# Optimization experiments

Hardware: AMD Instinct MI355X
Metric: run time of the kernel (lower is better)

Reference implementation:

```python
import jax, jax.numpy as jnp
import numpy as np

B, V, T, CIN, WEMB, H, NW = 32, 500, 24, 2, 4, 64, 8
C0 = CIN + WEMB  # 6 channels entering first layer


def _stglstm(x, supports, Wg, bg, Wo, bo, out_len=None, final_layer=False):
    # x: (B, C, V, T); supports: (S, V, V)
    Bb, C, Vv, Tt = x.shape
    T_steps = out_len if out_len is not None else Tt
    if final_layer:
        xs = jnp.broadcast_to(x[:, :, :, -1][None], (T_steps, Bb, C, Vv))
    else:
        xs = jnp.moveaxis(x, 3, 0)  # (T, B, C, V)

    def step(carry, xt):
        hx, cx = carry
        comb = xt + hx  # (B, C, V)
        feats = [comb]
        for s in range(supports.shape[0]):  # fixed small support_len loop
            x1 = jnp.einsum('bcv,vw->bcw', comb, supports[s])
            x2 = jnp.einsum('bcv,vw->bcw', x1, supports[s])
            feats += [x1, x2]  # order-2 diffusion
        g = jnp.concatenate(feats, axis=1)  # (B, 7C, V)
        gates = jnp.einsum('bgv,og->bov', g, Wg) + bg[None, :, None]  # (B, 4C, V)
        i, f, cg, o = jnp.split(gates, 4, axis=1)
        cy = jax.nn.sigmoid(f) * cx + jax.nn.sigmoid(i) * cg  # cellgate is linear (no tanh), as in source
        hy = jax.nn.sigmoid(o) * jnp.tanh(cy)
        return (hy, cy), hy

    h0 = jnp.zeros((Bb, C, Vv), x.dtype)
    _, hs = jax.lax.scan(step, (h0, h0), xs)  # hs: (T, B, C, V)
    hs = jnp.moveaxis(hs, 0, 3)  # (B, C, V, T)
    return jnp.einsum('bcvt,oc->bovt', hs, Wo) + bo[None, :, None, None]


def _se(x, Wa, Wb):
    y = x.mean(axis=(2, 3))  # (B, C) global avg pool
    y = jax.nn.sigmoid(jax.nn.relu(y @ Wa.T) @ Wb.T)
    return x * y[:, :, None, None]


def setup_inputs():
    key = jax.random.key(0)
    ks = jax.random.split(key, 24)

    def n(k, shape, s=0.05):
        return jax.random.normal(k, shape, jnp.float32) * s

    A = jax.random.uniform(ks[0], (3, V, V), jnp.float32)
    A = A / A.sum(-1, keepdims=True)  # row-stochastic random-walk matrices
    return {
        'x': n(ks[1], (B, CIN, V, T), 1.0),
        'supports': A,
        'w_type': jax.random.randint(ks[2], (B, V, T), 0, NW, dtype=jnp.int32),
        'Wemb': n(ks[3], (NW, WEMB)),
        'Wg0': n(ks[4], (4 * C0, 7 * C0)), 'bg0': jnp.zeros((4 * C0,), jnp.float32),
        'Wo0': n(ks[5], (H, C0)), 'bo0': jnp.zeros((H,), jnp.float32),
        'Ws0a': n(ks[6], (H // 16, H)), 'Ws0b': n(ks[7], (H, H // 16)),
        'Wg1': n(ks[8], (4 * H, 7 * H)), 'bg1': jnp.zeros((4 * H,), jnp.float32),
        'Wo1': n(ks[9], (H, H)), 'bo1': jnp.zeros((H,), jnp.float32),
        'Ws1a': n(ks[10], (H // 16, H)), 'Ws1b': n(ks[11], (H, H // 16)),
        'Wg2': n(ks[12], (4 * H, 7 * H)), 'bg2': jnp.zeros((4 * H,), jnp.float32),
        'Wo2': n(ks[13], (H, H)), 'bo2': jnp.zeros((H,), jnp.float32),
        'Wg3': n(ks[14], (4 * H, 7 * H)), 'bg3': jnp.zeros((4 * H,), jnp.float32),
        'Wo3': n(ks[15], (2, H)), 'bo3': jnp.zeros((2,), jnp.float32),
    }


def reference(x, supports, w_type, Wemb, Wg0, bg0, Wo0, bo0, Ws0a, Ws0b,
              Wg1, bg1, Wo1, bo1, Ws1a, Ws1b, Wg2, bg2, Wo2, bo2,
              Wg3, bg3, Wo3, bo3):
    w_vec = Wemb[w_type]  # (B, V, T, wemb)
    w_vec = jnp.transpose(w_vec, (0, 3, 1, 2))  # (B, wemb, V, T)
    h = jnp.concatenate([x, w_vec], axis=1)  # (B, CIN+wemb, V, T)
    h = _stglstm(h, supports, Wg0, bg0, Wo0, bo0)
    h = _se(h, Ws0a, Ws0b)
    h = _stglstm(h, supports, Wg1, bg1, Wo1, bo1)
    h = _se(h, Ws1a, Ws1b)
    h = _stglstm(h, supports, Wg2, bg2, Wo2, bo2)
    out = _stglstm(h, supports, Wg3, bg3, Wo3, bo3, out_len=T, final_layer=True)
    return out  # (B, 2, V, out_len)
```

## Files before the change

### kernel.cpp

```cpp
#include <hip/hip_runtime.h>
#include <math.h>

#define NV 500
#define NB 32
#define NT 24
#define NH 64

typedef _Float16 f16;
typedef _Float16 f16x8 __attribute__((ext_vector_type(8)));
typedef _Float16 f16x4 __attribute__((ext_vector_type(4)));
typedef float    f32x4 __attribute__((ext_vector_type(4)));

__device__ __forceinline__ float sigm(float x){ return 1.f/(1.f+expf(-x)); }

__global__ void k_a2(const float* __restrict__ A, float* __restrict__ A2)
{
    int idx = blockIdx.x*256 + threadIdx.x;
    if (idx >= 3*500*500) return;
    int wv = idx % 500; int rest = idx/500; int r = rest % 500; int s = rest/500;
    const float* Ar = A + ((size_t)s*500 + r)*500;
    const float* Ac = A + (size_t)s*500*500 + wv;
    float a = 0.f;
    for (int u = 0; u < 500; u++) a += Ar[u]*Ac[(size_t)u*500];
    A2[idx] = a;
}

__global__ void k_acat(const float* __restrict__ A, const float* __restrict__ A2,
                       f16* __restrict__ AcatT)
{
    int idx = blockIdx.x*256 + threadIdx.x;
    if (idx >= 3072*512) return;
    int k = idx & 511;
    int n = idx >> 9;
    int j = n >> 9, wv = n & 511;
    float val = 0.f;
    if (k < 500 && wv < 500) {
        int s = j >> 1;
        const float* M = (j & 1) ? A2 : A;
        val = M[((size_t)s*500 + k)*500 + wv];
    }
    AcatT[idx] = (f16)val;
}

__global__ void k_f2h(const float* __restrict__ src, f16* __restrict__ dst, int n)
{
    int idx = blockIdx.x*256 + threadIdx.x;
    if (idx < n) dst[idx] = (f16)src[idx];
}

__global__ __launch_bounds__(256)
void k_diff(const f16* __restrict__ Acv, const f16* __restrict__ Bt,
            f16* __restrict__ fout, int Mtot, int C, int G)
{
    __shared__ f16 lA[128*32];
    __shared__ f16 lB[128*32];
    const int tid = threadIdx.x;
    const int n0 = blockIdx.x*128, m0 = blockIdx.y*128;
    const int r0 = tid>>2, c0 = tid&3;
    const int swz0 = r0*32 + ((c0 ^ ((r0>>1)&3))<<3);
    const int swz1 = swz0 + 64*32;
    int mA0 = m0 + r0;      if (mA0 > Mtot-1) mA0 = Mtot-1;
    int mA1 = m0 + r0 + 64; if (mA1 > Mtot-1) mA1 = Mtot-1;
    const f16* gA0 = Acv + (size_t)mA0*512 + c0*8;
    const f16* gA1 = Acv + (size_t)mA1*512 + c0*8;
    const f16* gB0 = Bt + (size_t)(n0+r0)*512 + c0*8;
    const f16* gB1 = Bt + (size_t)(n0+r0+64)*512 + c0*8;

    const int w = tid>>6, lane = tid&63;
    const int wr = (w>>1)<<6, wc = (w&1)<<6;
    const int fm = lane&15, fk = lane>>4;
    const int fch = (fk ^ ((fm>>1)&3))<<3;

    f32x4 acc[4][4];
    #pragma unroll
    for (int i=0;i<4;i++)
        #pragma unroll
        for (int j=0;j<4;j++) acc[i][j] = (f32x4){0.f,0.f,0.f,0.f};

    f32x4 ra0 = *(const f32x4*)gA0, ra1 = *(const f32x4*)gA1;
    f32x4 rb0 = *(const f32x4*)gB0, rb1 = *(const f32x4*)gB1;

    for (int ks = 0; ks < 16; ks++) {
        __syncthreads();
        *(f32x4*)(lA + swz0) = ra0;  *(f32x4*)(lA + swz1) = ra1;
        *(f32x4*)(lB + swz0) = rb0;  *(f32x4*)(lB + swz1) = rb1;
        if (ks < 15) {
            int o = (ks+1)*32;
            ra0 = *(const f32x4*)(gA0 + o); ra1 = *(const f32x4*)(gA1 + o);
            rb0 = *(const f32x4*)(gB0 + o); rb1 = *(const f32x4*)(gB1 + o);
        }
        __syncthreads();
        f16x8 af[4], bf[4];
        #pragma unroll
        for (int i=0;i<4;i++) af[i] = *(const f16x8*)(lA + (wr + i*16 + fm)*32 + fch);
        #pragma unroll
        for (int j=0;j<4;j++) bf[j] = *(const f16x8*)(lB + (wc + j*16 + fm)*32 + fch);
        #pragma unroll
        for (int i=0;i<4;i++)
            #pragma unroll
            for (int j=0;j<4;j++)
                acc[i][j] = __builtin_amdgcn_mfma_f32_16x16x32_f16(af[i], bf[j], acc[i][j], 0, 0, 0);
    }

    #pragma unroll
    for (int j=0;j<4;j++) {
        int col = n0 + wc + j*16 + fm;
        int jb = col >> 9, wv = col & 511;
        if (wv >= 500) continue;
        #pragma unroll
        for (int i=0;i<4;i++) {
            int mb = m0 + wr + i*16 + fk*4;
            if (C == 64) {
                if (mb >= Mtot) continue;
                int b = mb >> 6, c = mb & 63;
                f16x4 h4;
                h4[0]=(f16)acc[i][j][0]; h4[1]=(f16)acc[i][j][1];
                h4[2]=(f16)acc[i][j][2]; h4[3]=(f16)acc[i][j][3];
                *(f16x4*)(fout + ((size_t)b*512 + wv)*G + C + jb*C + c) = h4;
            } else {
                #pragma unroll
                for (int r=0;r<4;r++) {
                    int m = mb + r;
                    if (m < Mtot) {
                        int b = m / C, c = m - b*C;
                        fout[((size_t)b*512 + wv)*G + C + jb*C + c] = (f16)acc[i][j][r];
                    }
                }
            }
        }
    }
}

__global__ __launch_bounds__(256)
void k_gateslstm(const f16* __restrict__ fT, const f16* __restrict__ Wg,
                 const float* __restrict__ bg, float* __restrict__ cst,
                 const f16* __restrict__ Xn, f16* __restrict__ hsave,
                 const float* __restrict__ Wo3, const float* __restrict__ bo3,
                 float* __restrict__ out, int t,
                 f16* __restrict__ fTout, f16* __restrict__ ccv,
                 int first, int writecomb)
{
    __shared__ f16 lA[64*32];
    __shared__ f16 lB[256*32];
    __shared__ float ExF[4*64*65];
    __shared__ float bgS[256];
    __shared__ f16 combS[64*68];
    const int tid = threadIdx.x;
    const int m0 = blockIdx.x*64, b = blockIdx.y;
    const f16* Ab = fT + (size_t)b*512*448;
    bgS[tid] = bg[tid];

    const int r0 = tid>>2, c0 = tid&3;
    const int swz = r0*32 + ((c0 ^ ((r0>>1)&3))<<3);
    const f16* gA = Ab + (size_t)(m0+r0)*448 + c0*8;
    const f16* gB = Wg + (size_t)r0*448 + c0*8;

    const int w = tid>>6, lane = tid&63;
    const int wc = w<<6;
    const int fm = lane&15, fk = lane>>4;
    const int fch = (fk ^ ((fm>>1)&3))<<3;

    f32x4 acc[4][4];
    #pragma unroll
    for (int i=0;i<4;i++)
        #pragma unroll
        for (int j=0;j<4;j++) acc[i][j] = (f32x4){0.f,0.f,0.f,0.f};

    f32x4 ra  = *(const f32x4*)gA;
    f32x4 rb0 = *(const f32x4*)gB;
    f32x4 rb1 = *(const f32x4*)(gB + (size_t)64*448);
    f32x4 rb2 = *(const f32x4*)(gB + (size_t)128*448);
    f32x4 rb3 = *(const f32x4*)(gB + (size_t)192*448);

    for (int ks = 0; ks < 14; ks++) {
        __syncthreads();
        *(f32x4*)(lA + swz) = ra;
        *(f32x4*)(lB + swz)          = rb0;
        *(f32x4*)(lB + 64*32 + swz)  = rb1;
        *(f32x4*)(lB + 128*32 + swz) = rb2;
        *(f32x4*)(lB + 192*32 + swz) = rb3;
        if (ks < 13) {
            int o = (ks+1)*32;
            ra  = *(const f32x4*)(gA + o);
            rb0 = *(const f32x4*)(gB + o);
            rb1 = *(const f32x4*)(gB + (size_t)64*448 + o);
            rb2 = *(const f32x4*)(gB + (size_t)128*448 + o);
            rb3 = *(const f32x4*)(gB + (size_t)192*448 + o);
        }
        __syncthreads();
        f16x8 af[4], bf[4];
        #pragma unroll
        for (int i=0;i<4;i++) af[i] = *(const f16x8*)(lA + (i*16 + fm)*32 + fch);
        #pragma unroll
        for (int j=0;j<4;j++) bf[j] = *(const f16x8*)(lB + (wc + j*16 + fm)*32 + fch);
        #pragma unroll
        for (int i=0;i<4;i++)
            #pragma unroll
            for (int j=0;j<4;j++)
                acc[i][j] = __builtin_amdgcn_mfma_f32_16x16x32_f16(af[i], bf[j], acc[i][j], 0, 0, 0);
    }

    __syncthreads();
    #pragma unroll
    for (int i=0;i<4;i++)
        #pragma unroll
        for (int j=0;j<4;j++)
            #pragma unroll
            for (int r=0;r<4;r++)
                ExF[((w<<6) + i*16 + (fk<<2) + r)*65 + (j<<4) + fm] = acc[i][j][r];
    __syncthreads();

    const int vl = tid>>2, p = tid&3;
    const int v = m0 + vl;
    const size_t row = (size_t)b*512 + v;
    float hy[16];
    float* cp = cst + row*64 + (p<<4);
    #pragma unroll
    for (int k4=0;k4<4;k4++) {
        f32x4 cx4 = first ? (f32x4){0.f,0.f,0.f,0.f} : *(const f32x4*)(cp + k4*4);
        f32x4 cy4;
        #pragma unroll
        for (int e=0;e<4;e++) {
            int c = (p<<4) + k4*4 + e;
            float gi = ExF[(         vl)*65 + c] + bgS[c];
            float gf = ExF[( 64 +    vl)*65 + c] + bgS[64+c];
            float gc = ExF[(128 +    vl)*65 + c] + bgS[128+c];
            float go = ExF[(192 +    vl)*65 + c] + bgS[192+c];
            float cy = sigm(gf)*cx4[e] + sigm(gi)*gc;
            cy4[e] = cy;
            hy[k4*4+e] = sigm(go)*tanhf(cy);
        }
        *(f32x4*)(cp + k4*4) = cy4;
    }

    if (hsave) {
        alignas(16) f16 tmp[16];
        #pragma unroll
        for (int k=0;k<16;k++) tmp[k] = (f16)hy[k];
        f16* hp = hsave + row*64 + (p<<4);
        *(f32x4*)hp = *(f32x4*)tmp;
        *(f32x4*)(hp+8) = *(f32x4*)(tmp+8);
    }

    if (out) {
        float r0s = 0.f, r1s = 0.f;
        #pragma unroll
        for (int k=0;k<16;k++){ r0s += Wo3[(p<<4)+k]*hy[k]; r1s += Wo3[64+(p<<4)+k]*hy[k]; }
        r0s += __shfl_xor(r0s, 1, 64); r0s += __shfl_xor(r0s, 2, 64);
        r1s += __shfl_xor(r1s, 1, 64); r1s += __shfl_xor(r1s, 2, 64);
        if (p == 0 && v < 500) {
            out[((size_t)(b*2+0)*500 + v)*24 + t] = r0s + bo3[0];
            out[((size_t)(b*2+1)*500 + v)*24 + t] = r1s + bo3[1];
        }
    }

    if (writecomb) {
        alignas(16) f16 c16[16];
        if (v < 500) {
            const f16* xp = Xn + row*64 + (p<<4);
            alignas(16) f16 xv[16];
            *(f32x4*)xv = *(const f32x4*)xp;
            *(f32x4*)(xv+8) = *(const f32x4*)(xp+8);
            #pragma unroll
            for (int k=0;k<16;k++) c16[k] = (f16)((float)xv[k] + hy[k]);
        } else {
            #pragma unroll
            for (int k=0;k<16;k++) c16[k] = (f16)0.f;
        }
        f16* fp = fTout + row*448 + (p<<4);
        *(f32x4*)fp = *(f32x4*)c16;
        *(f32x4*)(fp+8) = *(f32x4*)(c16+8);
        #pragma unroll
        for (int k=0;k<16;k++) combS[vl*68 + (p<<4) + k] = c16[k];
        __syncthreads();
        const int c = tid>>2, jj = tid&3;
        alignas(16) f16 tmp[16];
        #pragma unroll
        for (int k=0;k<16;k++) tmp[k] = combS[(jj*16+k)*68 + c];
        f16* dst = ccv + ((size_t)b*64 + c)*512 + m0 + jj*16;
        *(f32x4*)dst = *(f32x4*)tmp;
        *(f32x4*)(dst+8) = *(f32x4*)(tmp+8);
    }
}

__global__ __launch_bounds__(256)
void k_seed(const f16* __restrict__ X0, f16* __restrict__ fT, f16* __restrict__ ccv)
{
    __shared__ f16 combS[64*68];
    const int b = blockIdx.y, v0 = blockIdx.x*64;
    const int tid = threadIdx.x, vl = tid>>2, p = tid&3;
    const int v = v0 + vl;
    const size_t row = (size_t)b*512 + v;
    alignas(16) f16 c16[16];
    if (v < 500) {
        const f16* xp = X0 + row*64 + p*16;
        *(f32x4*)c16 = *(const f32x4*)xp;
        *(f32x4*)(c16+8) = *(const f32x4*)(xp+8);
    } else {
        #pragma unroll
        for (int k=0;k<16;k++) c16[k] = (f16)0.f;
    }
    f16* fp = fT + row*448 + p*16;
    *(f32x4*)fp = *(f32x4*)c16;
    *(f32x4*)(fp+8) = *(f32x4*)(c16+8);
    #pragma unroll
    for (int k=0;k<16;k++) combS[vl*68 + p*16 + k] = c16[k];
    __syncthreads();
    const int c = tid>>2, j = tid&3;
    alignas(16) f16 tmp[16];
    #pragma unroll
    for (int k=0;k<16;k++) tmp[k] = combS[(j*16+k)*68 + c];
    f16* dst = ccv + ((size_t)b*64 + c)*512 + v0 + j*16;
    *(f32x4*)dst = *(f32x4*)tmp;
    *(f32x4*)(dst+8) = *(f32x4*)(tmp+8);
}

__global__ __launch_bounds__(256)
void k_xprojm(const f16* __restrict__ src, const f16* __restrict__ WoF,
              const float* __restrict__ bo, const float* __restrict__ se,
              f16* __restrict__ X)
{
    __shared__ f16 lA[128*64];
    __shared__ f16 lB[64*64];
    const int tid = threadIdx.x;
    const size_t m0 = (size_t)blockIdx.x*128;
    const int r0 = tid>>2, c0 = tid&3;
    const int swz = r0*32 + ((c0 ^ ((r0>>1)&3))<<3);
    const f16* gA0 = src + (m0 + r0)*64 + c0*8;
    const f16* gA1 = gA0 + 64*64;
    const f16* gB  = WoF + r0*64 + c0*8;

    *(f32x4*)(lA + swz)               = *(const f32x4*)gA0;
    *(f32x4*)(lA + 2048 + swz)        = *(const f32x4*)gA1;
    *(f32x4*)(lA + 4096 + swz)        = *(const f32x4*)(gA0 + 32);
    *(f32x4*)(lA + 6144 + swz)        = *(const f32x4*)(gA1 + 32);
    *(f32x4*)(lB + swz)               = *(const f32x4*)gB;
    *(f32x4*)(lB + 2048 + swz)        = *(const f32x4*)(gB + 32);
    __syncthreads();

    const int w = tid>>6, lane = tid&63;
    const int wr = w<<5;
    const int fm = lane&15, fk = lane>>4;
    const int fch = (fk ^ ((fm>>1)&3))<<3;

    f32x4 acc[2][4];
    #pragma unroll
    for (int i=0;i<2;i++)
        #pragma unroll
        for (int j=0;j<4;j++) acc[i][j] = (f32x4){0.f,0.f,0.f,0.f};

    #pragma unroll
    for (int ks=0; ks<2; ks++) {
        f16x8 af[2], bf[4];
        #pragma unroll
        for (int i=0;i<2;i++) af[i] = *(const f16x8*)(lA + ks*4096 + (wr + i*16 + fm)*32 + fch);
        #pragma unroll
        for (int j=0;j<4;j++) bf[j] = *(const f16x8*)(lB + ks*2048 + (j*16 + fm)*32 + fch);
        #pragma unroll
        for (int i=0;i<2;i++)
            #pragma unroll
            for (int j=0;j<4;j++)
                acc[i][j] = __builtin_amdgcn_mfma_f32_16x16x32_f16(af[i], bf[j], acc[i][j], 0, 0, 0);
    }
    __syncthreads();

    const int bb = (int)((m0 >> 9) & 31);
    #pragma unroll
    for (int j=0;j<4;j++) {
        const int c = (j<<4) + fm;
        const float bias = bo[c];
        const float sf = se ? se[bb*64 + c] : 1.f;
        #pragma unroll
        for (int i=0;i<2;i++) {
            const int rbase = wr + i*16 + (fk<<2);
            #pragma unroll
            for (int r=0;r<4;r++)
                lA[(rbase + r)*64 + c] = (f16)(sf*(acc[i][j][r] + bias));
        }
    }
    __syncthreads();
    #pragma unroll
    for (int pass=0; pass<4; pass++) {
        int chunk = pass*256 + tid;
        int row = chunk>>3, off = (chunk&7)<<3;
        *(f32x4*)(X + (m0 + row)*64 + off) = *(const f32x4*)(lA + row*64 + off);
    }
}

__global__ void k_xproj1(const float* __restrict__ src, const float* __restrict__ Wo,
                         const float* __restrict__ bo, const float* __restrict__ se,
                         f16* __restrict__ X, int total)
{
    int id = blockIdx.x*256 + threadIdx.x;
    if (id >= total) return;
    int c = id & 63;
    size_t row = (size_t)(id >> 6);
    int b = (int)((row >> 9) & 31);
    const float* sp = src + row*6;
    float a = bo[c];
    #pragma unroll
    for (int j=0;j<6;j++) a += Wo[c*6+j]*sp[j];
    X[id] = (f16)(se[b*64+c]*a);
}

__global__ void k_xe(const float* __restrict__ x, const int* __restrict__ wt,
                     const float* __restrict__ Wemb, float* __restrict__ XE)
{
    int id = blockIdx.x*256 + threadIdx.x;
    if (id >= NT*NB*512) return;
    int v = id & 511; int r = id >> 9; int b = r & 31; int t = r >> 5;
    float vals[6] = {0.f,0.f,0.f,0.f,0.f,0.f};
    if (v < 500) {
        vals[0] = x[((size_t)(b*2+0)*500 + v)*24 + t];
        vals[1] = x[((size_t)(b*2+1)*500 + v)*24 + t];
        int wty = wt[((size_t)b*500 + v)*24 + t];
        vals[2] = Wemb[wty*4+0]; vals[3] = Wemb[wty*4+1];
        vals[4] = Wemb[wty*4+2]; vals[5] = Wemb[wty*4+3];
    }
    float* xe = XE + (size_t)id*6;
    #pragma unroll
    for (int c = 0; c < 6; c++) xe[c] = vals[c];
}

__global__ void k_seed0(const float* __restrict__ XE, f16* __restrict__ f0T,
                        f16* __restrict__ ccv0)
{
    int id = blockIdx.x*256 + threadIdx.x;
    if (id >= NB*512) return;
    int v = id & 511, b = id >> 9;
    const float* xe = XE + (size_t)id*6;
    #pragma unroll
    for (int c = 0; c < 6; c++) {
        f16 h = (v < 500) ? (f16)xe[c] : (f16)0.f;
        f0T[(size_t)id*42 + c] = h;
        ccv0[((size_t)b*6 + c)*512 + v] = h;
    }
}

__global__ __launch_bounds__(256)
void k_glstm0(f16* f0T, const float* __restrict__ Wg0,
              const float* __restrict__ bg0, float* __restrict__ cst0,
              float* __restrict__ hs0T, const float* __restrict__ XE,
              f16* __restrict__ ccv0, int t)
{
    __shared__ float WgS[24*42];
    __shared__ float bgS[24];
    int tid = threadIdx.x;
    for (int i = tid; i < 24*42; i += 256) WgS[i] = Wg0[i];
    if (tid < 24) bgS[tid] = bg0[tid];
    __syncthreads();
    int id = blockIdx.x*256 + tid;
    if (id >= NB*500) return;
    int b = id / 500, v = id - b*500;
    const f16* fp = f0T + ((size_t)b*512 + v)*42;
    float fv[42];
    #pragma unroll
    for (int g = 0; g < 42; g++) fv[g] = (float)fp[g];
    float gates[24];
    #pragma unroll
    for (int o = 0; o < 24; o++) {
        float a = bgS[o];
        #pragma unroll
        for (int g = 0; g < 42; g++) a += WgS[o*42+g]*fv[g];
        gates[o] = a;
    }
    size_t hrow = (((size_t)t*NB + b)*512 + v)*6;
    const float* xe = XE + (((size_t)(t+1)*NB + b)*512 + v)*6;
    #pragma unroll
    for (int c = 0; c < 6; c++) {
        size_t ci = ((size_t)b*500 + v)*6 + c;
        float cx = t ? cst0[ci] : 0.f;
        float cy = sigm(gates[6+c])*cx + sigm(gates[c])*gates[12+c];
        cst0[ci] = cy;
        float h = sigm(gates[18+c])*tanhf(cy);
        hs0T[hrow + c] = h;
        if (t < 23) {
            float cmb = xe[c] + h;
            f0T[((size_t)b*512 + v)*42 + c] = (f16)cmb;
            ccv0[((size_t)b*6 + c)*512 + v] = (f16)cmb;
        }
    }
}

__global__ void k_mean0(const float* __restrict__ hs0T, float* __restrict__ mean0)
{
    int b = blockIdx.x;
    float acc[6] = {0,0,0,0,0,0};
    for (int i = threadIdx.x; i < 24*500; i += 256) {
        int tt = i/500, v = i - tt*500;
        const float* p = hs0T + (((size_t)tt*NB + b)*512 + v)*6;
        #pragma unroll
        for (int c=0;c<6;c++) acc[c] += p[c];
    }
    __shared__ float red[256];
    for (int c=0;c<6;c++) {
        red[threadIdx.x] = acc[c]; __syncthreads();
        for (int s=128;s>0;s>>=1) { if (threadIdx.x<s) red[threadIdx.x]+=red[threadIdx.x+s]; __syncthreads(); }
        if (threadIdx.x==0) mean0[b*6+c] = red[0]/12000.f;
        __syncthreads();
    }
}

__global__ void k_mean1(const f16* __restrict__ hs1T, float* __restrict__ mean1)
{
    int cg = blockIdx.x, b = blockIdx.y;
    float acc[8] = {0,0,0,0,0,0,0,0};
    for (int i = threadIdx.x; i < 24*500; i += 256) {
        int tt = i/500, v = i - tt*500;
        const f16* p = hs1T + (((size_t)tt*NB + b)*512 + v)*64 + cg*8;
        #pragma unroll
        for (int c=0;c<8;c++) acc[c] += (float)p[c];
    }
    __shared__ float red[256];
    for (int c=0;c<8;c++) {
        red[threadIdx.x] = acc[c]; __syncthreads();
        for (int s=128;s>0;s>>=1) { if (threadIdx.x<s) red[threadIdx.x]+=red[threadIdx.x+s]; __syncthreads(); }
        if (threadIdx.x==0) mean1[b*64 + cg*8 + c] = red[0]/12000.f;
        __syncthreads();
    }
}

__global__ void k_se(const float* __restrict__ meanhs, const float* __restrict__ Wo,
                     const float* __restrict__ bo, int Cin,
                     const float* __restrict__ Wa, const float* __restrict__ Wb,
                     float* __restrict__ se)
{
    int b = blockIdx.x; int c = threadIdx.x;
    __shared__ float y[64]; __shared__ float a[4];
    float acc = bo[c];
    for (int j = 0; j < Cin; j++) acc += Wo[(size_t)c*Cin + j] * meanhs[b*Cin + j];
    y[c] = acc;
    __syncthreads();
    if (c < 4) {
        float s = 0.f;
        for (int j = 0; j < 64; j++) s += Wa[c*64 + j] * y[j];
        a[c] = fmaxf(s, 0.f);
    }
    __syncthreads();
    float s = 0.f;
    #pragma unroll
    for (int j = 0; j < 4; j++) s += Wb[c*4 + j] * a[j];
    se[b*64 + c] = 1.f/(1.f + expf(-s));
}

extern "C" void kernel_launch(void* const* d_in, const int* in_sizes, int n_in,
                              void* d_out, int out_size, void* d_ws, size_t ws_size,
                              hipStream_t stream)
{
    const float* x    = (const float*)d_in[0];
    const float* sup  = (const float*)d_in[1];
    const int*   wt   = (const int*)  d_in[2];
    const float* Wemb = (const float*)d_in[3];
    const float* Wg0  = (const float*)d_in[4];
    const float* bg0  = (const float*)d_in[5];
    const float* Wo0  = (const float*)d_in[6];
    const float* bo0  = (const float*)d_in[7];
    const float* Wa0  = (const float*)d_in[8];
    const float* Wb0  = (const float*)d_in[9];
    const float* Wg1  = (const float*)d_in[10];
    const float* bg1  = (const float*)d_in[11];
    const float* Wo1  = (const float*)d_in[12];
    const float* bo1  = (const float*)d_in[13];
    const float* Wa1  = (const float*)d_in[14];
    const float* Wb1  = (const float*)d_in[15];
    const float* Wg2  = (const float*)d_in[16];
    const float* bg2  = (const float*)d_in[17];
    const float* Wo2  = (const float*)d_in[18];
    const float* bo2  = (const float*)d_in[19];
    const float* Wg3  = (const float*)d_in[20];
    const float* bg3  = (const float*)d_in[21];
    const float* Wo3  = (const float*)d_in[22];
    const float* bo3  = (const float*)d_in[23];
    float* out = (float*)d_out;
    (void)in_sizes; (void)n_in; (void)out_size; (void)ws_size;

    char* ws = (char*)d_ws;
    size_t off = 0;
    f16*   AcatT  = (f16*)(ws + off);   off += (size_t)3072*512*2;
    float* A2     = (float*)(ws + off); off += (size_t)3*500*500*4;
    f16*   WgF1   = (f16*)(ws + off);   off += (size_t)256*448*2;
    f16*   WgF2   = (f16*)(ws + off);   off += (size_t)256*448*2;
    f16*   WgF3   = (f16*)(ws + off);   off += (size_t)256*448*2;
    f16*   WoF1   = (f16*)(ws + off);   off += (size_t)64*64*2;
    f16*   WoF2   = (f16*)(ws + off);   off += (size_t)64*64*2;
    f16*   comb_cv= (f16*)(ws + off);   off += (size_t)2048*512*2;
    f16*   ccv0   = (f16*)(ws + off);   off += (size_t)192*512*2;
    f16*   featsT = (f16*)(ws + off);   off += (size_t)NB*512*448*2;
    f16*   f0T    = (f16*)(ws + off);   off += (size_t)NB*512*42*2;
    float* XE     = (float*)(ws + off); off += (size_t)NT*NB*512*6*4;
    float* hs0T   = (float*)(ws + off); off += (size_t)NT*NB*512*6*4;
    f16*   hs1T   = (f16*)(ws + off);   off += (size_t)NT*NB*512*64*2;
    f16*   hT     = (f16*)(ws + off);   off += (size_t)NB*512*64*2;
    float* cstT   = (float*)(ws + off); off += (size_t)NB*512*64*4;
    float* cst0   = (float*)(ws + off); off += (size_t)NB*500*6*4;
    f16*   Xbuf   = (f16*)(ws + off);   off += (size_t)NT*NB*512*64*2;
    f16*   X3     = (f16*)(ws + off);   off += (size_t)NB*512*64*2;
    float* mean0  = (float*)(ws + off); off += 8192;
    float* se0    = (float*)(ws + off); off += 8192;
    float* mean1  = (float*)(ws + off); off += 8192;
    float* se1    = (float*)(ws + off); off += 8192;

    const size_t sliceH = (size_t)NB*512*64;

    k_a2  <<<(3*500*500 + 255)/256, 256, 0, stream>>>(sup, A2);
    k_acat<<<(3072*512 + 255)/256, 256, 0, stream>>>(sup, A2, AcatT);
    k_f2h <<<(256*448 + 255)/256, 256, 0, stream>>>(Wg1, WgF1, 256*448);
    k_f2h <<<(256*448 + 255)/256, 256, 0, stream>>>(Wg2, WgF2, 256*448);
    k_f2h <<<(256*448 + 255)/256, 256, 0, stream>>>(Wg3, WgF3, 256*448);
    k_f2h <<<16, 256, 0, stream>>>(Wo1, WoF1, 64*64);
    k_f2h <<<16, 256, 0, stream>>>(Wo2, WoF2, 64*64);
    k_xe  <<<(NT*NB*512)/256, 256, 0, stream>>>(x, wt, Wemb, XE);

    k_seed0<<<(NB*512)/256, 256, 0, stream>>>(XE, f0T, ccv0);
    for (int t = 0; t < NT; t++) {
        k_diff  <<<dim3(24, 2), 256, 0, stream>>>(ccv0, AcatT, f0T, 192, 6, 42);
        k_glstm0<<<(NB*500 + 255)/256, 256, 0, stream>>>(f0T, Wg0, bg0, cst0, hs0T, XE, ccv0, t);
    }
    k_mean0<<<NB, 256, 0, stream>>>(hs0T, mean0);
    k_se   <<<NB, 64, 0, stream>>>(mean0, Wo0, bo0, 6, Wa0, Wb0, se0);

    k_xproj1<<<(NT*NB*512*64)/256, 256, 0, stream>>>(hs0T, Wo0, bo0, se0, Xbuf, NT*NB*512*64);
    k_seed <<<dim3(8, NB), 256, 0, stream>>>(Xbuf, featsT, comb_cv);
    for (int t = 0; t < NT; t++) {
        k_diff <<<dim3(24, 16), 256, 0, stream>>>(comb_cv, AcatT, featsT, 2048, 64, 448);
        k_gateslstm<<<dim3(8, NB), 256, 0, stream>>>(featsT, WgF1, bg1, cstT,
                 (t < 23) ? Xbuf + (size_t)(t+1)*sliceH : (const f16*)nullptr,
                 hs1T + (size_t)t*sliceH, nullptr, nullptr, nullptr, t,
                 featsT, comb_cv, t == 0, t < 23);
    }
    k_mean1<<<dim3(8, NB), 256, 0, stream>>>(hs1T, mean1);
    k_se   <<<NB, 64, 0, stream>>>(mean1, Wo1, bo1, 64, Wa1, Wb1, se1);

    k_xprojm<<<(NT*NB*512)/128, 256, 0, stream>>>(hs1T, WoF1, bo1, se1, Xbuf);
    k_seed <<<dim3(8, NB), 256, 0, stream>>>(Xbuf, featsT, comb_cv);
    for (int t = 0; t < NT; t++) {
        k_diff <<<dim3(24, 16), 256, 0, stream>>>(comb_cv, AcatT, featsT, 2048, 64, 448);
        k_gateslstm<<<dim3(8, NB), 256, 0, stream>>>(featsT, WgF2, bg2, cstT,
                 (t < 23) ? Xbuf + (size_t)(t+1)*sliceH : (const f16*)nullptr,
                 (t == 23) ? hT : (f16*)nullptr, nullptr, nullptr, nullptr, t,
                 featsT, comb_cv, t == 0, t < 23);
    }

    k_xprojm<<<(NB*512)/128, 256, 0, stream>>>(hT, WoF2, bo2, nullptr, X3);
    k_seed <<<dim3(8, NB), 256, 0, stream>>>(X3, featsT, comb_cv);
    for (int t = 0; t < NT; t++) {
        k_diff <<<dim3(24, 16), 256, 0, stream>>>(comb_cv, AcatT, featsT, 2048, 64, 448);
        k_gateslstm<<<dim3(8, NB), 256, 0, stream>>>(featsT, WgF3, bg3, cstT,
                 X3, nullptr, Wo3, bo3, out, t,
                 featsT, comb_cv, t == 0, t < 23);
    }
}
```

Before: 4.593 ms.

## Fuse diffusion GEMM into gate LSTM kernel with ping-pong buffers, tile A2 precompute

Merges the per-step diffusion kernel and the gate/LSTM kernel into one k_step kernel. Each block computes its 64-node slice of the six diffused feature sets into shared memory, then runs the gate GEMM straight from LDS, so the 448-wide feature tensor no longer round-trips through global memory. This halves the launches per timestep, and ping-pong buffers for comb/ccv avoid read-write races across blocks. In exchange, each block recomputes diffusion over all 64 channels with only 256 blocks, which lowers parallelism compared with the separate 384-block diffusion kernel. Gate pre-activations are also staged in f16 rather than f32. The A^2 precompute is separately rewritten as a shared-memory tiled SGEMM.

```diff
diff --git a/kernel.cpp b/kernel.cpp
--- a/kernel.cpp
+++ b/kernel.cpp
@@ -13,16 +13,54 @@
 
 __device__ __forceinline__ float sigm(float x){ return 1.f/(1.f+expf(-x)); }
 
-__global__ void k_a2(const float* __restrict__ A, float* __restrict__ A2)
-{
-    int idx = blockIdx.x*256 + threadIdx.x;
-    if (idx >= 3*500*500) return;
-    int wv = idx % 500; int rest = idx/500; int r = rest % 500; int s = rest/500;
-    const float* Ar = A + ((size_t)s*500 + r)*500;
-    const float* Ac = A + (size_t)s*500*500 + wv;
-    float a = 0.f;
-    for (int u = 0; u < 500; u++) a += Ar[u]*Ac[(size_t)u*500];
-    A2[idx] = a;
+#define FID(v,g) ((((v)*448) + (g)) ^ (((v)&7)<<3))
+
+__global__ __launch_bounds__(256)
+void k_a2(const float* __restrict__ A, float* __restrict__ A2)
+{
+    __shared__ float tA[64][33];
+    __shared__ float tB[32][65];
+    const int s = blockIdx.z;
+    const int r0 = blockIdx.y*64, w0 = blockIdx.x*64;
+    const float* As = A + (size_t)s*500*500;
+    const int tid = threadIdx.x;
+    const int ty = tid>>4, tx = tid&15;
+    float acc[4][4] = {};
+    for (int k0 = 0; k0 < 500; k0 += 32) {
+        __syncthreads();
+        for (int e = tid; e < 64*32; e += 256) {
+            int r = e>>5, kk = e&31;
+            float v = 0.f;
+            if (r0+r < 500 && k0+kk < 500) v = As[(size_t)(r0+r)*500 + k0+kk];
+            tA[r][kk] = v;
+        }
+        for (int e = tid; e < 32*64; e += 256) {
+            int kk = e>>6, ww = e&63;
+            float v = 0.f;
+            if (k0+kk < 500 && w0+ww < 500) v = As[(size_t)(k0+kk)*500 + w0+ww];
+            tB[kk][ww] = v;
+        }
+        __syncthreads();
+        #pragma unroll 8
+        for (int kk = 0; kk < 32; kk++) {
+            float a0=tA[ty][kk], a1=tA[ty+16][kk], a2=tA[ty+32][kk], a3=tA[ty+48][kk];
+            float b0=tB[kk][tx], b1=tB[kk][tx+16], b2=tB[kk][tx+32], b3=tB[kk][tx+48];
+            acc[0][0]+=a0*b0; acc[0][1]+=a0*b1; acc[0][2]+=a0*b2; acc[0][3]+=a0*b3;
+            acc[1][0]+=a1*b0; acc[1][1]+=a1*b1; acc[1][2]+=a1*b2; acc[1][3]+=a1*b3;
+            acc[2][0]+=a2*b0; acc[2][1]+=a2*b1; acc[2][2]+=a2*b2; acc[2][3]+=a2*b3;
+            acc[3][0]+=a3*b0; acc[3][1]+=a3*b1; acc[3][2]+=a3*b2; acc[3][3]+=a3*b3;
+        }
+    }
+    #pragma unroll
+    for (int i=0;i<4;i++) {
+        int r = r0 + ty + 16*i;
+        if (r >= 500) continue;
+        #pragma unroll
+        for (int j=0;j<4;j++) {
+            int ww = w0 + tx + 16*j;
+            if (ww < 500) A2[((size_t)s*500 + r)*500 + ww] = acc[i][j];
+        }
+    }
 }
 
 __global__ void k_acat(const float* __restrict__ A, const float* __restrict__ A2,
@@ -110,21 +148,12 @@
         #pragma unroll
         for (int i=0;i<4;i++) {
             int mb = m0 + wr + i*16 + fk*4;
-            if (C == 64) {
-                if (mb >= Mtot) continue;
-                int b = mb >> 6, c = mb & 63;
-                f16x4 h4;
-                h4[0]=(f16)acc[i][j][0]; h4[1]=(f16)acc[i][j][1];
-                h4[2]=(f16)acc[i][j][2]; h4[3]=(f16)acc[i][j][3];
-                *(f16x4*)(fout + ((size_t)b*512 + wv)*G + C + jb*C + c) = h4;
-            } else {
-                #pragma unroll
-                for (int r=0;r<4;r++) {
-                    int m = mb + r;
-                    if (m < Mtot) {
-                        int b = m / C, c = m - b*C;
-                        fout[((size_t)b*512 + wv)*G + C + jb*C + c] = (f16)acc[i][j][r];
-                    }
+            #pragma unroll
+            for (int r=0;r<4;r++) {
+                int m = mb + r;
+                if (m < Mtot) {
+                    int b = m / C, c = m - b*C;
+                    fout[((size_t)b*512 + wv)*G + C + jb*C + c] = (f16)acc[i][j][r];
                 }
             }
         }
@@ -132,87 +161,156 @@
 }
 
 __global__ __launch_bounds__(256)
-void k_gateslstm(const f16* __restrict__ fT, const f16* __restrict__ Wg,
-                 const float* __restrict__ bg, float* __restrict__ cst,
-                 const f16* __restrict__ Xn, f16* __restrict__ hsave,
-                 const float* __restrict__ Wo3, const float* __restrict__ bo3,
-                 float* __restrict__ out, int t,
-                 f16* __restrict__ fTout, f16* __restrict__ ccv,
-                 int first, int writecomb)
-{
-    __shared__ f16 lA[64*32];
-    __shared__ f16 lB[256*32];
-    __shared__ float ExF[4*64*65];
-    __shared__ float bgS[256];
-    __shared__ f16 combS[64*68];
+void k_step(const f16* __restrict__ AcatT, const f16* __restrict__ ccv,
+            const f16* __restrict__ combV, const f16* __restrict__ Wg,
+            const float* __restrict__ bg, float* __restrict__ cst,
+            const f16* __restrict__ Xn, f16* __restrict__ hsave,
+            const float* __restrict__ Wo3, const float* __restrict__ bo3,
+            float* __restrict__ out, int t,
+            f16* __restrict__ ccv_out, f16* __restrict__ combV_out,
+            int first, int writecomb)
+{
+    __shared__ __align__(16) f16 SM[64*448 + 4096];
+    f16* feats = SM;
+    f16* stg   = SM + 64*448;
+    f16* lA = stg;
+    f16* lB = stg + 2048;
+
     const int tid = threadIdx.x;
-    const int m0 = blockIdx.x*64, b = blockIdx.y;
-    const f16* Ab = fT + (size_t)b*512*448;
-    bgS[tid] = bg[tid];
-
+    const int vt = blockIdx.x, b = blockIdx.y;
+    const int w = tid>>6, lane = tid&63;
+    const int fm = lane&15, fk = lane>>4;
+    const int fch = (fk ^ ((fm>>1)&3))<<3;
     const int r0 = tid>>2, c0 = tid&3;
     const int swz = r0*32 + ((c0 ^ ((r0>>1)&3))<<3);
-    const f16* gA = Ab + (size_t)(m0+r0)*448 + c0*8;
-    const f16* gB = Wg + (size_t)r0*448 + c0*8;
-
-    const int w = tid>>6, lane = tid&63;
-    const int wc = w<<6;
-    const int fm = lane&15, fk = lane>>4;
-    const int fch = (fk ^ ((fm>>1)&3))<<3;
-
-    f32x4 acc[4][4];
-    #pragma unroll
-    for (int i=0;i<4;i++)
-        #pragma unroll
-        for (int j=0;j<4;j++) acc[i][j] = (f32x4){0.f,0.f,0.f,0.f};
-
-    f32x4 ra  = *(const f32x4*)gA;
-    f32x4 rb0 = *(const f32x4*)gB;
-    f32x4 rb1 = *(const f32x4*)(gB + (size_t)64*448);
-    f32x4 rb2 = *(const f32x4*)(gB + (size_t)128*448);
-    f32x4 rb3 = *(const f32x4*)(gB + (size_t)192*448);
-
-    for (int ks = 0; ks < 14; ks++) {
-        __syncthreads();
-        *(f32x4*)(lA + swz) = ra;
-        *(f32x4*)(lB + swz)          = rb0;
-        *(f32x4*)(lB + 64*32 + swz)  = rb1;
-        *(f32x4*)(lB + 128*32 + swz) = rb2;
-        *(f32x4*)(lB + 192*32 + swz) = rb3;
-        if (ks < 13) {
-            int o = (ks+1)*32;
-            ra  = *(const f32x4*)(gA + o);
-            rb0 = *(const f32x4*)(gB + o);
-            rb1 = *(const f32x4*)(gB + (size_t)64*448 + o);
-            rb2 = *(const f32x4*)(gB + (size_t)128*448 + o);
-            rb3 = *(const f32x4*)(gB + (size_t)192*448 + o);
-        }
-        __syncthreads();
-        f16x8 af[4], bf[4];
-        #pragma unroll
-        for (int i=0;i<4;i++) af[i] = *(const f16x8*)(lA + (i*16 + fm)*32 + fch);
-        #pragma unroll
-        for (int j=0;j<4;j++) bf[j] = *(const f16x8*)(lB + (wc + j*16 + fm)*32 + fch);
-        #pragma unroll
-        for (int i=0;i<4;i++)
+    const int wrA = (w>>1)<<5;
+    const int wcA = (w&1)<<5;
+    const int wcB = (w&1)<<6;
+
+    {
+        int chunk = tid;
+        #pragma unroll
+        for (int pass=0; pass<2; pass++, chunk += 256) {
+            int v = chunk>>3, c8 = (chunk&7)<<3;
+            f32x4 d = *(const f32x4*)(combV + ((size_t)b*512 + vt*64 + v)*64 + c8);
+            *(f32x4*)(feats + FID(v, c8)) = d;
+        }
+    }
+
+    for (int jj = 0; jj < 6; jj++) {
+        const f16* gA = AcatT + ((size_t)(jj*512 + vt*64 + r0))*512 + c0*8;
+        const f16* gB = ccv + ((size_t)b*64 + r0)*512 + c0*8;
+        f32x4 ra = *(const f32x4*)gA;
+        f32x4 rb = *(const f32x4*)gB;
+        f32x4 acc[2][2];
+        #pragma unroll
+        for (int i=0;i<2;i++)
+            #pragma unroll
+            for (int j=0;j<2;j++) acc[i][j] = (f32x4){0.f,0.f,0.f,0.f};
+        for (int ks = 0; ks < 16; ks++) {
+            __syncthreads();
+            *(f32x4*)(lA + swz) = ra;
+            *(f32x4*)(lB + swz) = rb;
+            if (ks < 15) {
+                int o = (ks+1)*32;
+                ra = *(const f32x4*)(gA + o);
+                rb = *(const f32x4*)(gB + o);
+            }
+            __syncthreads();
+            f16x8 af[2], bf[2];
+            #pragma unroll
+            for (int i=0;i<2;i++) af[i] = *(const f16x8*)(lA + (wrA + i*16 + fm)*32 + fch);
+            #pragma unroll
+            for (int j=0;j<2;j++) bf[j] = *(const f16x8*)(lB + (wcA + j*16 + fm)*32 + fch);
+            #pragma unroll
+            for (int i=0;i<2;i++)
+                #pragma unroll
+                for (int j=0;j<2;j++)
+                    acc[i][j] = __builtin_amdgcn_mfma_f32_16x16x32_f16(af[i], bf[j], acc[i][j], 0, 0, 0);
+        }
+        #pragma unroll
+        for (int i=0;i<2;i++)
+            #pragma unroll
+            for (int j=0;j<2;j++)
+                #pragma unroll
+                for (int rr=0;rr<4;rr++) {
+                    int v = wrA + i*16 + (fk<<2) + rr;
+                    int g = 64 + jj*64 + wcA + j*16 + fm;
+                    feats[FID(v, g)] = (f16)acc[i][j][rr];
+                }
+    }
+    __syncthreads();
+
+    f32x4 acch[2][2][4];
+    #pragma unroll
+    for (int h = 0; h < 2; h++) {
+        const f16* gW0 = Wg + ((size_t)(h*128 + r0))*448 + c0*8;
+        const f16* gW1 = gW0 + (size_t)64*448;
+        f32x4 rw0 = *(const f32x4*)gW0;
+        f32x4 rw1 = *(const f32x4*)gW1;
+        f32x4 acc[2][4];
+        #pragma unroll
+        for (int i=0;i<2;i++)
+            #pragma unroll
+            for (int j=0;j<4;j++) acc[i][j] = (f32x4){0.f,0.f,0.f,0.f};
+        for (int ks = 0; ks < 14; ks++) {
+            __syncthreads();
+            *(f32x4*)(stg + swz) = rw0;
+            *(f32x4*)(stg + 64*32 + swz) = rw1;
+            if (ks < 13) {
+                int o = (ks+1)*32;
+                rw0 = *(const f32x4*)(gW0 + o);
+                rw1 = *(const f32x4*)(gW1 + o);
+            }
+            __syncthreads();
+            f16x8 af[2], bf[4];
+            #pragma unroll
+            for (int i=0;i<2;i++) {
+                int m = wrA + i*16 + fm;
+                af[i] = *(const f16x8*)(feats + FID(m, ks*32 + (fk<<3)));
+            }
+            #pragma unroll
+            for (int j=0;j<4;j++) bf[j] = *(const f16x8*)(stg + (wcB + j*16 + fm)*32 + fch);
+            #pragma unroll
+            for (int i=0;i<2;i++)
+                #pragma unroll
+                for (int j=0;j<4;j++)
+                    acc[i][j] = __builtin_amdgcn_mfma_f32_16x16x32_f16(af[i], bf[j], acc[i][j], 0, 0, 0);
+        }
+        #pragma unroll
+        for (int i=0;i<2;i++)
+            #pragma unroll
+            for (int j=0;j<4;j++) acch[h][i][j] = acc[i][j];
+    }
+    __syncthreads();
+
+    f16* ExF = SM;
+    #pragma unroll
+    for (int h=0;h<2;h++) {
+        const int q = h*2 + (w&1);
+        #pragma unroll
+        for (int i=0;i<2;i++)
             #pragma unroll
             for (int j=0;j<4;j++)
-                acc[i][j] = __builtin_amdgcn_mfma_f32_16x16x32_f16(af[i], bf[j], acc[i][j], 0, 0, 0);
-    }
-
-    __syncthreads();
-    #pragma unroll
-    for (int i=0;i<4;i++)
-        #pragma unroll
-        for (int j=0;j<4;j++)
-            #pragma unroll
-            for (int r=0;r<4;r++)
-                ExF[((w<<6) + i*16 + (fk<<2) + r)*65 + (j<<4) + fm] = acc[i][j][r];
+                #pragma unroll
+                for (int rr=0;rr<4;rr++) {
+                    int v = wrA + i*16 + (fk<<2) + rr;
+                    int c = j*16 + fm;
+                    ExF[((((q<<6)+v)<<6) + c) ^ ((v&7)<<3)] = (f16)acch[h][i][j][rr];
+                }
+    }
     __syncthreads();
 
     const int vl = tid>>2, p = tid&3;
-    const int v = m0 + vl;
+    const int v = vt*64 + vl;
     const size_t row = (size_t)b*512 + v;
+    alignas(16) f16 gq[4][16];
+    #pragma unroll
+    for (int q=0;q<4;q++) {
+        int base = (((q<<6)+vl)<<6) + (p<<4);
+        *(f32x4*)&gq[q][0] = *(const f32x4*)(ExF + (base ^ ((vl&7)<<3)));
+        *(f32x4*)&gq[q][8] = *(const f32x4*)(ExF + ((base+8) ^ ((vl&7)<<3)));
+    }
     float hy[16];
     float* cp = cst + row*64 + (p<<4);
     #pragma unroll
@@ -221,14 +319,14 @@
         f32x4 cy4;
         #pragma unroll
         for (int e=0;e<4;e++) {
-            int c = (p<<4) + k4*4 + e;
-            float gi = ExF[(         vl)*65 + c] + bgS[c];
-            float gf = ExF[( 64 +    vl)*65 + c] + bgS[64+c];
-            float gc = ExF[(128 +    vl)*65 + c] + bgS[128+c];
-            float go = ExF[(192 +    vl)*65 + c] + bgS[192+c];
-            float cy = sigm(gf)*cx4[e] + sigm(gi)*gc;
+            int kk = k4*4+e, c = (p<<4) + kk;
+            float gi = (float)gq[0][kk] + bg[c];
+            float gf = (float)gq[1][kk] + bg[64+c];
+            float gcv= (float)gq[2][kk] + bg[128+c];
+            float go = (float)gq[3][kk] + bg[192+c];
+            float cy = sigm(gf)*cx4[e] + sigm(gi)*gcv;
             cy4[e] = cy;
-            hy[k4*4+e] = sigm(go)*tanhf(cy);
+            hy[kk] = sigm(go)*tanhf(cy);
         }
         *(f32x4*)(cp + k4*4) = cy4;
     }
@@ -255,6 +353,7 @@
     }
 
     if (writecomb) {
+        f16* combS = SM + 16384;
         alignas(16) f16 c16[16];
         if (v < 500) {
             const f16* xp = Xn + row*64 + (p<<4);
@@ -267,24 +366,23 @@
             #pragma unroll
             for (int k=0;k<16;k++) c16[k] = (f16)0.f;
         }
-        f16* fp = fTout + row*448 + (p<<4);
-        *(f32x4*)fp = *(f32x4*)c16;
-        *(f32x4*)(fp+8) = *(f32x4*)(c16+8);
+        *(f32x4*)(combV_out + row*64 + (p<<4)) = *(f32x4*)c16;
+        *(f32x4*)(combV_out + row*64 + (p<<4) + 8) = *(f32x4*)(c16+8);
         #pragma unroll
         for (int k=0;k<16;k++) combS[vl*68 + (p<<4) + k] = c16[k];
         __syncthreads();
-        const int c = tid>>2, jj = tid&3;
+        const int cc = tid>>2, jj2 = tid&3;
         alignas(16) f16 tmp[16];
         #pragma unroll
-        for (int k=0;k<16;k++) tmp[k] = combS[(jj*16+k)*68 + c];
-        f16* dst = ccv + ((size_t)b*64 + c)*512 + m0 + jj*16;
+        for (int k=0;k<16;k++) tmp[k] = combS[(jj2*16+k)*68 + cc];
+        f16* dst = ccv_out + ((size_t)b*64 + cc)*512 + vt*64 + jj2*16;
         *(f32x4*)dst = *(f32x4*)tmp;
         *(f32x4*)(dst+8) = *(f32x4*)(tmp+8);
     }
 }
 
 __global__ __launch_bounds__(256)
-void k_seed(const f16* __restrict__ X0, f16* __restrict__ fT, f16* __restrict__ ccv)
+void k_seed(const f16* __restrict__ X0, f16* __restrict__ ccv, f16* __restrict__ combV)
 {
     __shared__ f16 combS[64*68];
     const int b = blockIdx.y, v0 = blockIdx.x*64;
@@ -300,9 +398,8 @@
         #pragma unroll
         for (int k=0;k<16;k++) c16[k] = (f16)0.f;
     }
-    f16* fp = fT + row*448 + p*16;
-    *(f32x4*)fp = *(f32x4*)c16;
-    *(f32x4*)(fp+8) = *(f32x4*)(c16+8);
+    *(f32x4*)(combV + row*64 + p*16) = *(f32x4*)c16;
+    *(f32x4*)(combV + row*64 + p*16 + 8) = *(f32x4*)(c16+8);
     #pragma unroll
     for (int k=0;k<16;k++) combS[vl*68 + p*16 + k] = c16[k];
     __syncthreads();
@@ -583,9 +680,11 @@
     f16*   WgF3   = (f16*)(ws + off);   off += (size_t)256*448*2;
     f16*   WoF1   = (f16*)(ws + off);   off += (size_t)64*64*2;
     f16*   WoF2   = (f16*)(ws + off);   off += (size_t)64*64*2;
-    f16*   comb_cv= (f16*)(ws + off);   off += (size_t)2048*512*2;
+    f16*   ccvP0  = (f16*)(ws + off);   off += (size_t)2048*512*2;
+    f16*   ccvP1  = (f16*)(ws + off);   off += (size_t)2048*512*2;
+    f16*   combV0 = (f16*)(ws + off);   off += (size_t)NB*512*64*2;
+    f16*   combV1 = (f16*)(ws + off);   off += (size_t)NB*512*64*2;
     f16*   ccv0   = (f16*)(ws + off);   off += (size_t)192*512*2;
-    f16*   featsT = (f16*)(ws + off);   off += (size_t)NB*512*448*2;
     f16*   f0T    = (f16*)(ws + off);   off += (size_t)NB*512*42*2;
     float* XE     = (float*)(ws + off); off += (size_t)NT*NB*512*6*4;
     float* hs0T   = (float*)(ws + off); off += (size_t)NT*NB*512*6*4;
@@ -602,7 +701,7 @@
 
     const size_t sliceH = (size_t)NB*512*64;
 
-    k_a2  <<<(3*500*500 + 255)/256, 256, 0, stream>>>(sup, A2);
+    k_a2  <<<dim3(8, 8, 3), 256, 0, stream>>>(sup, A2);
     k_acat<<<(3072*512 + 255)/256, 256, 0, stream>>>(sup, A2, AcatT);
     k_f2h <<<(256*448 + 255)/256, 256, 0, stream>>>(Wg1, WgF1, 256*448);
     k_f2h <<<(256*448 + 255)/256, 256, 0, stream>>>(Wg2, WgF2, 256*448);
@@ -620,33 +719,42 @@
     k_se   <<<NB, 64, 0, stream>>>(mean0, Wo0, bo0, 6, Wa0, Wb0, se0);
 
     k_xproj1<<<(NT*NB*512*64)/256, 256, 0, stream>>>(hs0T, Wo0, bo0, se0, Xbuf, NT*NB*512*64);
-    k_seed <<<dim3(8, NB), 256, 0, stream>>>(Xbuf, featsT, comb_cv);
+    k_seed <<<dim3(8, NB), 256, 0, stream>>>(Xbuf, ccvP0, combV0);
     for (int t = 0; t < NT; t++) {
-        k_diff <<<dim3(24, 16), 256, 0, stream>>>(comb_cv, AcatT, featsT, 2048, 64, 448);
-        k_gateslstm<<<dim3(8, NB), 256, 0, stream>>>(featsT, WgF1, bg1, cstT,
+        f16* ccvR  = (t & 1) ? ccvP1  : ccvP0;
+        f16* ccvW  = (t & 1) ? ccvP0  : ccvP1;
+        f16* cvR   = (t & 1) ? combV1 : combV0;
+        f16* cvW   = (t & 1) ? combV0 : combV1;
+        k_step<<<dim3(8, NB), 256, 0, stream>>>(AcatT, ccvR, cvR, WgF1, bg1, cstT,
                  (t < 23) ? Xbuf + (size_t)(t+1)*sliceH : (const f16*)nullptr,
                  hs1T + (size_t)t*sliceH, nullptr, nullptr, nullptr, t,
-                 featsT, comb_cv, t == 0, t < 23);
+                 ccvW, cvW, t == 0, t < 23);
     }
     k_mean1<<<dim3(8, NB), 256, 0, stream>>>(hs1T, mean1);
     k_se   <<<NB, 64, 0, stream>>>(mean1, Wo1, bo1, 64, Wa1, Wb1, se1);
 
     k_xprojm<<<(NT*NB*512)/128, 256, 0, stream>>>(hs1T, WoF1, bo1, se1, Xbuf);
-    k_seed <<<dim3(8, NB), 256, 0, stream>>>(Xbuf, featsT, comb_cv);
+    k_seed <<<dim3(8, NB), 256, 0, stream>>>(Xbuf, ccvP0, combV0);
     for (int t = 0; t < NT; t++) {
-        k_diff <<<dim3(24, 16), 256, 0, stream>>>(comb_cv, AcatT, featsT, 2048, 64, 448);
-        k_gateslstm<<<dim3(8, NB), 256, 0, stream>>>(featsT, WgF2, bg2, cstT,
+        f16* ccvR  = (t & 1) ? ccvP1  : ccvP0;
+        f16* ccvW  = (t & 1) ? ccvP0  : ccvP1;
+        f16* cvR   = (t & 1) ? combV1 : combV0;
+        f16* cvW   = (t & 1) ? combV0 : combV1;
+        k_step<<<dim3(8, NB), 256, 0, stream>>>(AcatT, ccvR, cvR, WgF2, bg2, cstT,
                  (t < 23) ? Xbuf + (size_t)(t+1)*sliceH : (const f16*)nullptr,
                  (t == 23) ? hT : (f16*)nullptr, nullptr, nullptr, nullptr, t,
-                 featsT, comb_cv, t == 0, t < 23);
+                 ccvW, cvW, t == 0, t < 23);
     }
 
     k_xprojm<<<(NB*512)/128, 256, 0, stream>>>(hT, WoF2, bo2, nullptr, X3);
-    k_seed <<<dim3(8, NB), 256, 0, stream>>>(X3, featsT, comb_cv);
+    k_seed <<<dim3(8, NB), 256, 0, stream>>>(X3, ccvP0, combV0);
     for (int t = 0; t < NT; t++) {
-        k_diff <<<dim3(24, 16), 256, 0, stream>>>(comb_cv, AcatT, featsT, 2048, 64, 448);
-        k_gateslstm<<<dim3(8, NB), 256, 0, stream>>>(featsT, WgF3, bg3, cstT,
+        f16* ccvR  = (t & 1) ? ccvP1  : ccvP0;
+        f16* ccvW  = (t & 1) ? ccvP0  : ccvP1;
+        f16* cvR   = (t & 1) ? combV1 : combV0;
+        f16* cvW   = (t & 1) ? combV0 : combV1;
+        k_step<<<dim3(8, NB), 256, 0, stream>>>(AcatT, ccvR, cvR, WgF3, bg3, cstT,
                  X3, nullptr, Wo3, bo3, out, t,
-                 featsT, comb_cv, t == 0, t < 23);
-    }
-}
+                 ccvW, cvW, t == 0, t < 23);
+    }
+}
```

Result: slower. 5.284 ms (+15.0%).
